# Kernel tuning notes

Hardware: AMD Instinct MI355X
Metric: run time of the kernel (lower is better)

The kernel has to match this reference:

```python
import jax, jax.numpy as jnp
import numpy as np

NUM_NODES = 4096
IN_DIM = 16
HIDDEN = 64
OUT_DIM = 32
HEADS = 4
NEG_SLOPE = 0.2
NEG_INF = -1e9


def _glorot(key, shape):
    fan_in, fan_out = shape[0], shape[-1]
    lim = jnp.sqrt(6.0 / (fan_in + fan_out))
    return jax.random.uniform(key, shape, jnp.float32, -lim, lim)


def setup_inputs() -> dict:
    key = jax.random.key(0)
    ks = jax.random.split(key, 8)
    B = 2
    return {
        "x": jax.random.normal(ks[0], (B, NUM_NODES, IN_DIM), jnp.float32),
        "embedding": _glorot(ks[1], (NUM_NODES, HIDDEN)),
        "W_proj": _glorot(ks[2], (IN_DIM, HIDDEN)),
        "b_proj": jnp.zeros((HIDDEN,), jnp.float32),
        "W1": _glorot(ks[3], (HIDDEN, HIDDEN)),  # heads=4, 16 per head, concat -> 64
        "att1_src": _glorot(ks[4], (HEADS, HIDDEN // HEADS)),
        "att1_dst": _glorot(ks[5], (HEADS, HIDDEN // HEADS)),
        "b1": jnp.zeros((HIDDEN,), jnp.float32),
        "W2": _glorot(ks[6], (HIDDEN, OUT_DIM)),  # heads=4, 8 per head, concat -> 32
        "att2_src": _glorot(ks[7], (HEADS, OUT_DIM // HEADS)),
        "att2_dst": _glorot(jax.random.fold_in(key, 99), (HEADS, OUT_DIM // HEADS)),
        "b2": jnp.zeros((OUT_DIM,), jnp.float32),
    }


def _gat(x, mask, W, a_src, a_dst, b):
    """Dense masked GAT layer. x: [B,N,Fin], mask: [N,N] bool (shared over batch).

    Equivalent to GATConv over edge list tf.where(adj > 0.5): for each target i,
    softmax over neighbors j of LeakyReLU(a_dst.Wh_i + a_src.Wh_j), aggregate Wh_j.
    """
    B, N, _ = x.shape
    H, F = a_src.shape
    h = (x @ W).reshape(B, N, H, F)                       # [B,N,H,F]
    s_src = jnp.einsum('bnhf,hf->bnh', h, a_src)          # per-source score
    s_dst = jnp.einsum('bnhf,hf->bnh', h, a_dst)          # per-target score
    e = s_dst[:, :, None, :] + s_src[:, None, :, :]       # [B,i,j,H]
    e = jnp.where(e > 0, e, NEG_SLOPE * e)                # LeakyReLU(0.2)
    e = jnp.where(mask[None, :, :, None], e, NEG_INF)
    alpha = jax.nn.softmax(e, axis=2)                     # softmax over neighbors j
    out = jnp.einsum('bijh,bjhf->bihf', alpha, h).reshape(B, N, H * F)
    return out + b


def reference(x, embedding, W_proj, b_proj, W1, att1_src, att1_dst, b1,
              W2, att2_src, att2_dst, b2):
    # AdaptiveAdjacency: cosine similarity of l2-normalized node embeddings
    ne = embedding / jnp.linalg.norm(embedding, axis=-1, keepdims=True)
    adj = ne @ ne.T                                       # [N,N], same for all batch
    mask = adj > 0.5                                      # edge set (incl. self-loops)

    h = x @ W_proj + b_proj                               # Dense proj -> hidden
    h = jax.nn.relu(_gat(h, mask, W1, att1_src, att1_dst, b1))
    return _gat(h, mask, W2, att2_src, att2_dst, b2)
```

## Files before the change

### kernel.cpp

```cpp
#include <hip/hip_runtime.h>
#include <hip/hip_bf16.h>
#include <stdint.h>

#define N_NODES 4096
#define BATCH 2

typedef __attribute__((ext_vector_type(8))) short short8v;
typedef __attribute__((ext_vector_type(4))) float f32x4;

#define GLL16(gsrc, ldst) \
    __builtin_amdgcn_global_load_lds((const __attribute__((address_space(1))) void*)(gsrc), \
                                     (__attribute__((address_space(3))) void*)(ldst), 16, 0, 0)

static __device__ inline unsigned short f2bf_rn(float x) {
    unsigned u = __float_as_uint(x);
    unsigned r = (u + 0x7FFFu + ((u >> 16) & 1u)) >> 16;
    return (unsigned short)r;
}
static __device__ inline float bf2f(unsigned short b) {
    return __uint_as_float(((unsigned)b) << 16);
}
static __device__ inline float rl(float v, int k) {
    return __uint_as_float(__builtin_amdgcn_readlane(__float_as_uint(v), k));
}

__global__ __launch_bounds__(64) void norm_kernel(const float* __restrict__ emb,
                                                  unsigned short* __restrict__ hi,
                                                  unsigned short* __restrict__ lo) {
    int row = blockIdx.x;
    int l = threadIdx.x;
    float v = emb[row * 64 + l];
    float s = v * v;
#pragma unroll
    for (int m = 32; m >= 1; m >>= 1) s += __shfl_xor(s, m);
    float nv = v / sqrtf(s);
    unsigned short h = f2bf_rn(nv);
    unsigned short lw = f2bf_rn(nv - bf2f(h));
    hi[row * 64 + l] = h;
    lo[row * 64 + l] = lw;
}

__global__ __launch_bounds__(256) void adj_mfma_kernel(
        const unsigned short* __restrict__ hi, const unsigned short* __restrict__ lo,
        unsigned long long* __restrict__ mask) {
    __shared__ unsigned short Ah[128 * 64];
    __shared__ unsigned short Al[128 * 64];
    __shared__ unsigned short Bh[128 * 64];
    __shared__ unsigned short Bl[128 * 64];
    int t = threadIdx.x;
    int w = t >> 6, l = t & 63;
    int i0 = blockIdx.y * 128, j0 = blockIdx.x * 128;

    int cr = l >> 3;
    int slot = (l & 7) ^ cr;
#pragma unroll
    for (int q = 0; q < 4; ++q) {
        int lr = w * 32 + q * 8;
        size_t ga = (size_t)(i0 + lr + cr) * 64 + slot * 8;
        size_t gb = (size_t)(j0 + lr + cr) * 64 + slot * 8;
        GLL16(hi + ga, &Ah[lr * 64]);
        GLL16(lo + ga, &Al[lr * 64]);
        GLL16(hi + gb, &Bh[lr * 64]);
        GLL16(lo + gb, &Bl[lr * 64]);
    }
    __syncthreads();

    int fr = l & 15;
    int s0 = l >> 4;
    int r7 = l & 7;
    short8v aH[2][2], aL[2][2];
#pragma unroll
    for (int rt = 0; rt < 2; ++rt) {
        int base = (w * 32 + rt * 16 + fr) * 64;
        aH[rt][0] = *(const short8v*)&Ah[base + ((s0 ^ r7) << 3)];
        aH[rt][1] = *(const short8v*)&Ah[base + (((s0 + 4) ^ r7) << 3)];
        aL[rt][0] = *(const short8v*)&Al[base + ((s0 ^ r7) << 3)];
        aL[rt][1] = *(const short8v*)&Al[base + (((s0 + 4) ^ r7) << 3)];
    }

    f32x4 acc[2][8];
#pragma unroll
    for (int rt = 0; rt < 2; ++rt)
#pragma unroll
        for (int js = 0; js < 8; ++js) acc[rt][js] = (f32x4){0.f, 0.f, 0.f, 0.f};

#pragma unroll
    for (int js = 0; js < 8; ++js) {
        int bbase = (js * 16 + fr) * 64;
        short8v bH0 = *(const short8v*)&Bh[bbase + ((s0 ^ r7) << 3)];
        short8v bH1 = *(const short8v*)&Bh[bbase + (((s0 + 4) ^ r7) << 3)];
        short8v bL0 = *(const short8v*)&Bl[bbase + ((s0 ^ r7) << 3)];
        short8v bL1 = *(const short8v*)&Bl[bbase + (((s0 + 4) ^ r7) << 3)];
#pragma unroll
        for (int rt = 0; rt < 2; ++rt) {
            f32x4 a = acc[rt][js];
            a = __builtin_amdgcn_mfma_f32_16x16x32_bf16(aH[rt][0], bH0, a, 0, 0, 0);
            a = __builtin_amdgcn_mfma_f32_16x16x32_bf16(aH[rt][1], bH1, a, 0, 0, 0);
            a = __builtin_amdgcn_mfma_f32_16x16x32_bf16(aH[rt][0], bL0, a, 0, 0, 0);
            a = __builtin_amdgcn_mfma_f32_16x16x32_bf16(aH[rt][1], bL1, a, 0, 0, 0);
            a = __builtin_amdgcn_mfma_f32_16x16x32_bf16(aL[rt][0], bH0, a, 0, 0, 0);
            a = __builtin_amdgcn_mfma_f32_16x16x32_bf16(aL[rt][1], bH1, a, 0, 0, 0);
            acc[rt][js] = a;
        }
    }

    int shift = ((l & 15) >> 2) * 16;
    int r = l & 3;
#pragma unroll
    for (int rt = 0; rt < 2; ++rt) {
#pragma unroll
        for (int ws_ = 0; ws_ < 2; ++ws_) {
            unsigned long long w64 = 0;
#pragma unroll
            for (int js2 = 0; js2 < 4; ++js2) {
                f32x4 a = acc[rt][ws_ * 4 + js2];
                unsigned long long b0 = __ballot(a[0] > 0.5f);
                unsigned long long b1 = __ballot(a[1] > 0.5f);
                unsigned long long b2 = __ballot(a[2] > 0.5f);
                unsigned long long b3 = __ballot(a[3] > 0.5f);
                unsigned long long sel = r == 0 ? b0 : r == 1 ? b1 : r == 2 ? b2 : b3;
                w64 |= ((sel >> shift) & 0xFFFFULL) << (js2 * 16);
            }
            if (l < 16)
                mask[(size_t)(i0 + w * 32 + rt * 16 + l) * 64 + blockIdx.x * 2 + ws_] = w64;
        }
    }
}

__global__ __launch_bounds__(256) void feat1_kernel(
        const float* __restrict__ x, const float* __restrict__ Wp,
        const float* __restrict__ bp, const float* __restrict__ W1,
        const float* __restrict__ a1s, const float* __restrict__ a1d,
        float* __restrict__ h1out, float* __restrict__ ssrc, float* __restrict__ sdst) {
    int w = threadIdx.x >> 6, l = threadIdx.x & 63;
    int row0 = blockIdx.x * 16 + w * 4;

    float xv[4];
#pragma unroll
    for (int r = 0; r < 4; ++r) xv[r] = x[(size_t)(row0 + r) * 16 + (l & 15)];

    float h0[4];
    float bpv = bp[l];
#pragma unroll
    for (int r = 0; r < 4; ++r) h0[r] = bpv;
#pragma unroll
    for (int k = 0; k < 16; ++k) {
        float wk = Wp[k * 64 + l];
#pragma unroll
        for (int r = 0; r < 4; ++r) h0[r] += rl(xv[r], k) * wk;
    }

    float h1[4] = {0.f, 0.f, 0.f, 0.f};
#pragma unroll
    for (int k = 0; k < 64; ++k) {
        float wk = W1[k * 64 + l];
#pragma unroll
        for (int r = 0; r < 4; ++r) h1[r] += rl(h0[r], k) * wk;
    }

    float as_ = a1s[l], ad_ = a1d[l];
#pragma unroll
    for (int r = 0; r < 4; ++r) {
        h1out[(size_t)(row0 + r) * 64 + l] = h1[r];
        float ps = h1[r] * as_, pd = h1[r] * ad_;
#pragma unroll
        for (int m = 8; m >= 1; m >>= 1) {
            ps += __shfl_xor(ps, m);
            pd += __shfl_xor(pd, m);
        }
        if ((l & 15) == 0) {
            ssrc[(size_t)(row0 + r) * 4 + (l >> 4)] = ps;
            sdst[(size_t)(row0 + r) * 4 + (l >> 4)] = pd;
        }
    }
}

__global__ __launch_bounds__(64) void agg1_fused_kernel(
        const float* __restrict__ h1, const float* __restrict__ ssrc,
        const float* __restrict__ sdst, const unsigned long long* __restrict__ mask,
        const float* __restrict__ b1, const float* __restrict__ W2,
        const float* __restrict__ a2s, const float* __restrict__ a2d,
        float* __restrict__ h2out, float* __restrict__ s2s, float* __restrict__ s2d) {
    int row = blockIdx.x;
    int i = row & (N_NODES - 1);
    int bN = row - i;
    int t = threadIdx.x;
    int hh = t >> 4;

    float sd = sdst[(size_t)row * 4 + hh];
    unsigned long long myword = mask[(size_t)i * 64 + t];

    float m = -1e30f, denom = 0.f, acc = 0.f;
    unsigned long long nz = __ballot(myword != 0ULL);
    while (nz) {
        int lw = __ffsll(nz) - 1;
        nz &= nz - 1;
        unsigned long long wbits = __shfl(myword, lw);
        while (wbits) {
            int bpos = __ffsll(wbits) - 1;
            wbits &= wbits - 1;
            int j = (lw << 6) + bpos;
            float e = sd + ssrc[(size_t)(bN + j) * 4 + hh];
            e = e > 0.f ? e : 0.2f * e;
            float mn = fmaxf(m, e);
            float cf = __expf(m - mn);
            float wg = __expf(e - mn);
            float hv = h1[(size_t)(bN + j) * 64 + t];
            denom = denom * cf + wg;
            acc = acc * cf + wg * hv;
            m = mn;
        }
    }
    float o = fmaxf(acc / denom + b1[t], 0.f);

    int l2 = t & 31;
    float acc2 = 0.f;
#pragma unroll
    for (int k = 0; k < 64; ++k) acc2 += rl(o, k) * W2[k * 32 + l2];

    float ps = acc2 * a2s[l2], pd = acc2 * a2d[l2];
#pragma unroll
    for (int mm = 4; mm >= 1; mm >>= 1) {
        ps += __shfl_xor(ps, mm);
        pd += __shfl_xor(pd, mm);
    }
    if (t < 32) {
        h2out[(size_t)row * 32 + t] = acc2;
        if ((t & 7) == 0) {
            s2s[(size_t)row * 4 + (t >> 3)] = ps;
            s2d[(size_t)row * 4 + (t >> 3)] = pd;
        }
    }
}

template <int HID, int F, int RELU>
__global__ __launch_bounds__(64) void gat_agg_kernel(
        const float* __restrict__ hfeat, const float* __restrict__ ssrc,
        const float* __restrict__ sdst, const unsigned long long* __restrict__ mask,
        const float* __restrict__ bias, float* __restrict__ out) {
    int row = blockIdx.x;
    int i = row & (N_NODES - 1);
    int bN = row - i;
    int t = threadIdx.x;
    int tt = t & (HID - 1);
    int hh = tt / F;

    float sd = sdst[(size_t)row * 4 + hh];
    unsigned long long myword = mask[(size_t)i * 64 + t];

    float m = -1e30f, denom = 0.f, acc = 0.f;
    unsigned long long nz = __ballot(myword != 0ULL);
    while (nz) {
        int lw = __ffsll(nz) - 1;
        nz &= nz - 1;
        unsigned long long wbits = __shfl(myword, lw);
        while (wbits) {
            int bpos = __ffsll(wbits) - 1;
            wbits &= wbits - 1;
            int j = (lw << 6) + bpos;
            float e = sd + ssrc[(size_t)(bN + j) * 4 + hh];
            e = e > 0.f ? e : 0.2f * e;
            float mn = fmaxf(m, e);
            float cf = __expf(m - mn);
            float wg = __expf(e - mn);
            float hv = hfeat[(size_t)(bN + j) * HID + tt];
            denom = denom * cf + wg;
            acc = acc * cf + wg * hv;
            m = mn;
        }
    }
    float o = acc / denom + bias[tt];
    if (RELU) o = fmaxf(o, 0.f);
    if (t < HID) out[(size_t)row * HID + tt] = o;
}

extern "C" void kernel_launch(void* const* d_in, const int* in_sizes, int n_in,
                              void* d_out, int out_size, void* d_ws, size_t ws_size,
                              hipStream_t stream) {
    const float* x   = (const float*)d_in[0];
    const float* emb = (const float*)d_in[1];
    const float* Wp  = (const float*)d_in[2];
    const float* bp  = (const float*)d_in[3];
    const float* W1  = (const float*)d_in[4];
    const float* a1s = (const float*)d_in[5];
    const float* a1d = (const float*)d_in[6];
    const float* b1  = (const float*)d_in[7];
    const float* W2  = (const float*)d_in[8];
    const float* a2s = (const float*)d_in[9];
    const float* a2d = (const float*)d_in[10];
    const float* b2  = (const float*)d_in[11];

    const int ROWS = BATCH * N_NODES;

    char* w = (char*)d_ws;
    unsigned short* ne_hi = (unsigned short*)w;  w += (size_t)N_NODES * 64 * 2;
    unsigned short* ne_lo = (unsigned short*)w;  w += (size_t)N_NODES * 64 * 2;
    unsigned long long* mask = (unsigned long long*)w; w += (size_t)N_NODES * 64 * 8;
    float* h1  = (float*)w;                      w += (size_t)ROWS * 64 * 4;
    float* s1s = (float*)w;                      w += (size_t)ROWS * 4 * 4;
    float* s1d = (float*)w;                      w += (size_t)ROWS * 4 * 4;
    float* h2  = (float*)w;                      w += (size_t)ROWS * 32 * 4;
    float* s2s = (float*)w;                      w += (size_t)ROWS * 4 * 4;
    float* s2d = (float*)w;                      w += (size_t)ROWS * 4 * 4;

    norm_kernel<<<dim3(N_NODES), dim3(64), 0, stream>>>(emb, ne_hi, ne_lo);
    adj_mfma_kernel<<<dim3(32, 32), dim3(256), 0, stream>>>(ne_hi, ne_lo, mask);
    feat1_kernel<<<dim3(ROWS / 16), dim3(256), 0, stream>>>(
        x, Wp, bp, W1, a1s, a1d, h1, s1s, s1d);
    agg1_fused_kernel<<<dim3(ROWS), dim3(64), 0, stream>>>(
        h1, s1s, s1d, mask, b1, W2, a2s, a2d, h2, s2s, s2d);
    gat_agg_kernel<32, 8, 0><<<dim3(ROWS), dim3(64), 0, stream>>>(
        h2, s2s, s2d, mask, b2, (float*)d_out);
}
```

Baseline: 39.06 us.

## Fuse normalization into adjacency kernel and co-launch feature projection blocks

```diff
diff --git a/kernel.cpp b/kernel.cpp
--- a/kernel.cpp
+++ b/kernel.cpp
@@ -6,11 +6,8 @@
 #define BATCH 2
 
 typedef __attribute__((ext_vector_type(8))) short short8v;
+typedef __attribute__((ext_vector_type(4))) unsigned short ushort4v;
 typedef __attribute__((ext_vector_type(4))) float f32x4;
-
-#define GLL16(gsrc, ldst) \
-    __builtin_amdgcn_global_load_lds((const __attribute__((address_space(1))) void*)(gsrc), \
-                                     (__attribute__((address_space(3))) void*)(ldst), 16, 0, 0)
 
 static __device__ inline unsigned short f2bf_rn(float x) {
     unsigned u = __float_as_uint(x);
@@ -24,167 +21,170 @@
     return __uint_as_float(__builtin_amdgcn_readlane(__float_as_uint(v), k));
 }
 
-__global__ __launch_bounds__(64) void norm_kernel(const float* __restrict__ emb,
-                                                  unsigned short* __restrict__ hi,
-                                                  unsigned short* __restrict__ lo) {
-    int row = blockIdx.x;
-    int l = threadIdx.x;
-    float v = emb[row * 64 + l];
-    float s = v * v;
-#pragma unroll
-    for (int m = 32; m >= 1; m >>= 1) s += __shfl_xor(s, m);
-    float nv = v / sqrtf(s);
-    unsigned short h = f2bf_rn(nv);
-    unsigned short lw = f2bf_rn(nv - bf2f(h));
-    hi[row * 64 + l] = h;
-    lo[row * 64 + l] = lw;
-}
-
-__global__ __launch_bounds__(256) void adj_mfma_kernel(
-        const unsigned short* __restrict__ hi, const unsigned short* __restrict__ lo,
-        unsigned long long* __restrict__ mask) {
+__global__ __launch_bounds__(256) void k1_kernel(
+        const float* __restrict__ emb, unsigned long long* __restrict__ mask,
+        const float* __restrict__ x, const float* __restrict__ Wp,
+        const float* __restrict__ bp, const float* __restrict__ W1,
+        const float* __restrict__ a1s, const float* __restrict__ a1d,
+        float* __restrict__ h1out, float* __restrict__ ssrc, float* __restrict__ sdst) {
     __shared__ unsigned short Ah[128 * 64];
     __shared__ unsigned short Al[128 * 64];
     __shared__ unsigned short Bh[128 * 64];
     __shared__ unsigned short Bl[128 * 64];
     int t = threadIdx.x;
-    int w = t >> 6, l = t & 63;
-    int i0 = blockIdx.y * 128, j0 = blockIdx.x * 128;
-
-    int cr = l >> 3;
-    int slot = (l & 7) ^ cr;
-#pragma unroll
-    for (int q = 0; q < 4; ++q) {
-        int lr = w * 32 + q * 8;
-        size_t ga = (size_t)(i0 + lr + cr) * 64 + slot * 8;
-        size_t gb = (size_t)(j0 + lr + cr) * 64 + slot * 8;
-        GLL16(hi + ga, &Ah[lr * 64]);
-        GLL16(lo + ga, &Al[lr * 64]);
-        GLL16(hi + gb, &Bh[lr * 64]);
-        GLL16(lo + gb, &Bl[lr * 64]);
-    }
-    __syncthreads();
-
-    int fr = l & 15;
-    int s0 = l >> 4;
-    int r7 = l & 7;
-    short8v aH[2][2], aL[2][2];
-#pragma unroll
-    for (int rt = 0; rt < 2; ++rt) {
-        int base = (w * 32 + rt * 16 + fr) * 64;
-        aH[rt][0] = *(const short8v*)&Ah[base + ((s0 ^ r7) << 3)];
-        aH[rt][1] = *(const short8v*)&Ah[base + (((s0 + 4) ^ r7) << 3)];
-        aL[rt][0] = *(const short8v*)&Al[base + ((s0 ^ r7) << 3)];
-        aL[rt][1] = *(const short8v*)&Al[base + (((s0 + 4) ^ r7) << 3)];
-    }
-
-    f32x4 acc[2][8];
-#pragma unroll
-    for (int rt = 0; rt < 2; ++rt)
-#pragma unroll
-        for (int js = 0; js < 8; ++js) acc[rt][js] = (f32x4){0.f, 0.f, 0.f, 0.f};
-
-#pragma unroll
-    for (int js = 0; js < 8; ++js) {
-        int bbase = (js * 16 + fr) * 64;
-        short8v bH0 = *(const short8v*)&Bh[bbase + ((s0 ^ r7) << 3)];
-        short8v bH1 = *(const short8v*)&Bh[bbase + (((s0 + 4) ^ r7) << 3)];
-        short8v bL0 = *(const short8v*)&Bl[bbase + ((s0 ^ r7) << 3)];
-        short8v bL1 = *(const short8v*)&Bl[bbase + (((s0 + 4) ^ r7) << 3)];
+
+    if (blockIdx.x < 1024) {
+        int bi = blockIdx.x >> 5, bj = blockIdx.x & 31;
+        int i0 = bi * 128, j0 = bj * 128;
+        int w = t >> 6, l = t & 63;
+
+        int l16 = t & 15;
+        int s8 = l16 >> 1, hf = l16 & 1;
+#pragma unroll
+        for (int it = 0; it < 8; ++it) {
+            int r = it * 16 + (t >> 4);
+            float4 av = *(const float4*)&emb[(size_t)(i0 + r) * 64 + l16 * 4];
+            float4 bv = *(const float4*)&emb[(size_t)(j0 + r) * 64 + l16 * 4];
+            float sa = av.x * av.x + av.y * av.y + av.z * av.z + av.w * av.w;
+            float sb = bv.x * bv.x + bv.y * bv.y + bv.z * bv.z + bv.w * bv.w;
+#pragma unroll
+            for (int m = 8; m >= 1; m >>= 1) {
+                sa += __shfl_xor(sa, m);
+                sb += __shfl_xor(sb, m);
+            }
+            float ia = 1.f / sqrtf(sa), ib = 1.f / sqrtf(sb);
+            float a0 = av.x * ia, a1 = av.y * ia, a2 = av.z * ia, a3 = av.w * ia;
+            float b0 = bv.x * ib, b1 = bv.y * ib, b2 = bv.z * ib, b3 = bv.w * ib;
+            ushort4v ah = {f2bf_rn(a0), f2bf_rn(a1), f2bf_rn(a2), f2bf_rn(a3)};
+            ushort4v bh = {f2bf_rn(b0), f2bf_rn(b1), f2bf_rn(b2), f2bf_rn(b3)};
+            ushort4v al = {f2bf_rn(a0 - bf2f(ah.x)), f2bf_rn(a1 - bf2f(ah.y)),
+                           f2bf_rn(a2 - bf2f(ah.z)), f2bf_rn(a3 - bf2f(ah.w))};
+            ushort4v bl = {f2bf_rn(b0 - bf2f(bh.x)), f2bf_rn(b1 - bf2f(bh.y)),
+                           f2bf_rn(b2 - bf2f(bh.z)), f2bf_rn(b3 - bf2f(bh.w))};
+            int si = r * 64 + ((s8 ^ (r & 7)) << 3) + hf * 4;
+            *(ushort4v*)&Ah[si] = ah;
+            *(ushort4v*)&Al[si] = al;
+            *(ushort4v*)&Bh[si] = bh;
+            *(ushort4v*)&Bl[si] = bl;
+        }
+        __syncthreads();
+
+        int fr = l & 15;
+        int s0 = l >> 4;
+        int r7 = l & 7;
+        short8v aH[2][2], aL[2][2];
 #pragma unroll
         for (int rt = 0; rt < 2; ++rt) {
-            f32x4 a = acc[rt][js];
-            a = __builtin_amdgcn_mfma_f32_16x16x32_bf16(aH[rt][0], bH0, a, 0, 0, 0);
-            a = __builtin_amdgcn_mfma_f32_16x16x32_bf16(aH[rt][1], bH1, a, 0, 0, 0);
-            a = __builtin_amdgcn_mfma_f32_16x16x32_bf16(aH[rt][0], bL0, a, 0, 0, 0);
-            a = __builtin_amdgcn_mfma_f32_16x16x32_bf16(aH[rt][1], bL1, a, 0, 0, 0);
-            a = __builtin_amdgcn_mfma_f32_16x16x32_bf16(aL[rt][0], bH0, a, 0, 0, 0);
-            a = __builtin_amdgcn_mfma_f32_16x16x32_bf16(aL[rt][1], bH1, a, 0, 0, 0);
-            acc[rt][js] = a;
-        }
-    }
-
-    int shift = ((l & 15) >> 2) * 16;
-    int r = l & 3;
-#pragma unroll
-    for (int rt = 0; rt < 2; ++rt) {
-#pragma unroll
-        for (int ws_ = 0; ws_ < 2; ++ws_) {
-            unsigned long long w64 = 0;
-#pragma unroll
-            for (int js2 = 0; js2 < 4; ++js2) {
-                f32x4 a = acc[rt][ws_ * 4 + js2];
-                unsigned long long b0 = __ballot(a[0] > 0.5f);
-                unsigned long long b1 = __ballot(a[1] > 0.5f);
-                unsigned long long b2 = __ballot(a[2] > 0.5f);
-                unsigned long long b3 = __ballot(a[3] > 0.5f);
-                unsigned long long sel = r == 0 ? b0 : r == 1 ? b1 : r == 2 ? b2 : b3;
-                w64 |= ((sel >> shift) & 0xFFFFULL) << (js2 * 16);
-            }
-            if (l < 16)
-                mask[(size_t)(i0 + w * 32 + rt * 16 + l) * 64 + blockIdx.x * 2 + ws_] = w64;
-        }
-    }
-}
-
-__global__ __launch_bounds__(256) void feat1_kernel(
-        const float* __restrict__ x, const float* __restrict__ Wp,
-        const float* __restrict__ bp, const float* __restrict__ W1,
-        const float* __restrict__ a1s, const float* __restrict__ a1d,
-        float* __restrict__ h1out, float* __restrict__ ssrc, float* __restrict__ sdst) {
-    int w = threadIdx.x >> 6, l = threadIdx.x & 63;
-    int row0 = blockIdx.x * 16 + w * 4;
-
-    float xv[4];
-#pragma unroll
-    for (int r = 0; r < 4; ++r) xv[r] = x[(size_t)(row0 + r) * 16 + (l & 15)];
-
-    float h0[4];
-    float bpv = bp[l];
-#pragma unroll
-    for (int r = 0; r < 4; ++r) h0[r] = bpv;
-#pragma unroll
-    for (int k = 0; k < 16; ++k) {
-        float wk = Wp[k * 64 + l];
-#pragma unroll
-        for (int r = 0; r < 4; ++r) h0[r] += rl(xv[r], k) * wk;
-    }
-
-    float h1[4] = {0.f, 0.f, 0.f, 0.f};
-#pragma unroll
-    for (int k = 0; k < 64; ++k) {
-        float wk = W1[k * 64 + l];
-#pragma unroll
-        for (int r = 0; r < 4; ++r) h1[r] += rl(h0[r], k) * wk;
-    }
-
-    float as_ = a1s[l], ad_ = a1d[l];
-#pragma unroll
-    for (int r = 0; r < 4; ++r) {
-        h1out[(size_t)(row0 + r) * 64 + l] = h1[r];
-        float ps = h1[r] * as_, pd = h1[r] * ad_;
-#pragma unroll
-        for (int m = 8; m >= 1; m >>= 1) {
-            ps += __shfl_xor(ps, m);
-            pd += __shfl_xor(pd, m);
-        }
-        if ((l & 15) == 0) {
-            ssrc[(size_t)(row0 + r) * 4 + (l >> 4)] = ps;
-            sdst[(size_t)(row0 + r) * 4 + (l >> 4)] = pd;
-        }
-    }
-}
-
-__global__ __launch_bounds__(64) void agg1_fused_kernel(
+            int base = (w * 32 + rt * 16 + fr) * 64;
+            aH[rt][0] = *(const short8v*)&Ah[base + ((s0 ^ r7) << 3)];
+            aH[rt][1] = *(const short8v*)&Ah[base + (((s0 + 4) ^ r7) << 3)];
+            aL[rt][0] = *(const short8v*)&Al[base + ((s0 ^ r7) << 3)];
+            aL[rt][1] = *(const short8v*)&Al[base + (((s0 + 4) ^ r7) << 3)];
+        }
+
+        f32x4 acc[2][8];
+#pragma unroll
+        for (int rt = 0; rt < 2; ++rt)
+#pragma unroll
+            for (int js = 0; js < 8; ++js) acc[rt][js] = (f32x4){0.f, 0.f, 0.f, 0.f};
+
+#pragma unroll
+        for (int js = 0; js < 8; ++js) {
+            int bbase = (js * 16 + fr) * 64;
+            short8v bH0 = *(const short8v*)&Bh[bbase + ((s0 ^ r7) << 3)];
+            short8v bH1 = *(const short8v*)&Bh[bbase + (((s0 + 4) ^ r7) << 3)];
+            short8v bL0 = *(const short8v*)&Bl[bbase + ((s0 ^ r7) << 3)];
+            short8v bL1 = *(const short8v*)&Bl[bbase + (((s0 + 4) ^ r7) << 3)];
+#pragma unroll
+            for (int rt = 0; rt < 2; ++rt) {
+                f32x4 a = acc[rt][js];
+                a = __builtin_amdgcn_mfma_f32_16x16x32_bf16(aH[rt][0], bH0, a, 0, 0, 0);
+                a = __builtin_amdgcn_mfma_f32_16x16x32_bf16(aH[rt][1], bH1, a, 0, 0, 0);
+                a = __builtin_amdgcn_mfma_f32_16x16x32_bf16(aH[rt][0], bL0, a, 0, 0, 0);
+                a = __builtin_amdgcn_mfma_f32_16x16x32_bf16(aH[rt][1], bL1, a, 0, 0, 0);
+                a = __builtin_amdgcn_mfma_f32_16x16x32_bf16(aL[rt][0], bH0, a, 0, 0, 0);
+                a = __builtin_amdgcn_mfma_f32_16x16x32_bf16(aL[rt][1], bH1, a, 0, 0, 0);
+                acc[rt][js] = a;
+            }
+        }
+
+        int shift = ((l & 15) >> 2) * 16;
+        int r = l & 3;
+#pragma unroll
+        for (int rt = 0; rt < 2; ++rt) {
+#pragma unroll
+            for (int ws_ = 0; ws_ < 2; ++ws_) {
+                unsigned long long w64 = 0;
+#pragma unroll
+                for (int js2 = 0; js2 < 4; ++js2) {
+                    f32x4 a = acc[rt][ws_ * 4 + js2];
+                    unsigned long long c0 = __ballot(a[0] > 0.5f);
+                    unsigned long long c1 = __ballot(a[1] > 0.5f);
+                    unsigned long long c2 = __ballot(a[2] > 0.5f);
+                    unsigned long long c3 = __ballot(a[3] > 0.5f);
+                    unsigned long long sel = r == 0 ? c0 : r == 1 ? c1 : r == 2 ? c2 : c3;
+                    w64 |= ((sel >> shift) & 0xFFFFULL) << (js2 * 16);
+                }
+                if (l < 16)
+                    mask[(size_t)(i0 + w * 32 + rt * 16 + l) * 64 + bj * 2 + ws_] = w64;
+            }
+        }
+    } else {
+        int b = blockIdx.x - 1024;
+        int w = t >> 6, l = t & 63;
+        int row0 = b * 32 + w * 8;
+
+        float xv[8];
+#pragma unroll
+        for (int r = 0; r < 8; ++r) xv[r] = x[(size_t)(row0 + r) * 16 + (l & 15)];
+
+        float h0[8];
+        float bpv = bp[l];
+#pragma unroll
+        for (int r = 0; r < 8; ++r) h0[r] = bpv;
+#pragma unroll
+        for (int k = 0; k < 16; ++k) {
+            float wk = Wp[k * 64 + l];
+#pragma unroll
+            for (int r = 0; r < 8; ++r) h0[r] += rl(xv[r], k) * wk;
+        }
+
+        float h1[8] = {0.f, 0.f, 0.f, 0.f, 0.f, 0.f, 0.f, 0.f};
+#pragma unroll
+        for (int k = 0; k < 64; ++k) {
+            float wk = W1[k * 64 + l];
+#pragma unroll
+            for (int r = 0; r < 8; ++r) h1[r] += rl(h0[r], k) * wk;
+        }
+
+        float as_ = a1s[l], ad_ = a1d[l];
+#pragma unroll
+        for (int r = 0; r < 8; ++r) {
+            h1out[(size_t)(row0 + r) * 64 + l] = h1[r];
+            float ps = h1[r] * as_, pd = h1[r] * ad_;
+#pragma unroll
+            for (int m = 8; m >= 1; m >>= 1) {
+                ps += __shfl_xor(ps, m);
+                pd += __shfl_xor(pd, m);
+            }
+            if ((l & 15) == 0) {
+                ssrc[(size_t)(row0 + r) * 4 + (l >> 4)] = ps;
+                sdst[(size_t)(row0 + r) * 4 + (l >> 4)] = pd;
+            }
+        }
+    }
+}
+
+__global__ __launch_bounds__(256) void agg1_fused_kernel(
         const float* __restrict__ h1, const float* __restrict__ ssrc,
         const float* __restrict__ sdst, const unsigned long long* __restrict__ mask,
         const float* __restrict__ b1, const float* __restrict__ W2,
         const float* __restrict__ a2s, const float* __restrict__ a2d,
         float* __restrict__ h2out, float* __restrict__ s2s, float* __restrict__ s2d) {
-    int row = blockIdx.x;
+    int row = blockIdx.x * 4 + (threadIdx.x >> 6);
     int i = row & (N_NODES - 1);
     int bN = row - i;
-    int t = threadIdx.x;
+    int t = threadIdx.x & 63;
     int hh = t >> 4;
 
     float sd = sdst[(size_t)row * 4 + hh];
@@ -233,17 +233,16 @@
     }
 }
 
-template <int HID, int F, int RELU>
-__global__ __launch_bounds__(64) void gat_agg_kernel(
+__global__ __launch_bounds__(256) void agg2_kernel(
         const float* __restrict__ hfeat, const float* __restrict__ ssrc,
         const float* __restrict__ sdst, const unsigned long long* __restrict__ mask,
         const float* __restrict__ bias, float* __restrict__ out) {
-    int row = blockIdx.x;
+    int row = blockIdx.x * 4 + (threadIdx.x >> 6);
     int i = row & (N_NODES - 1);
     int bN = row - i;
-    int t = threadIdx.x;
-    int tt = t & (HID - 1);
-    int hh = tt / F;
+    int t = threadIdx.x & 63;
+    int tt = t & 31;
+    int hh = tt >> 3;
 
     float sd = sdst[(size_t)row * 4 + hh];
     unsigned long long myword = mask[(size_t)i * 64 + t];
@@ -263,15 +262,14 @@
             float mn = fmaxf(m, e);
             float cf = __expf(m - mn);
             float wg = __expf(e - mn);
-            float hv = hfeat[(size_t)(bN + j) * HID + tt];
+            float hv = hfeat[(size_t)(bN + j) * 32 + tt];
             denom = denom * cf + wg;
             acc = acc * cf + wg * hv;
             m = mn;
         }
     }
     float o = acc / denom + bias[tt];
-    if (RELU) o = fmaxf(o, 0.f);
-    if (t < HID) out[(size_t)row * HID + tt] = o;
+    if (t < 32) out[(size_t)row * 32 + tt] = o;
 }
 
 extern "C" void kernel_launch(void* const* d_in, const int* in_sizes, int n_in,
@@ -293,8 +291,6 @@
     const int ROWS = BATCH * N_NODES;
 
     char* w = (char*)d_ws;
-    unsigned short* ne_hi = (unsigned short*)w;  w += (size_t)N_NODES * 64 * 2;
-    unsigned short* ne_lo = (unsigned short*)w;  w += (size_t)N_NODES * 64 * 2;
     unsigned long long* mask = (unsigned long long*)w; w += (size_t)N_NODES * 64 * 8;
     float* h1  = (float*)w;                      w += (size_t)ROWS * 64 * 4;
     float* s1s = (float*)w;                      w += (size_t)ROWS * 4 * 4;
@@ -303,12 +299,10 @@
     float* s2s = (float*)w;                      w += (size_t)ROWS * 4 * 4;
     float* s2d = (float*)w;                      w += (size_t)ROWS * 4 * 4;
 
-    norm_kernel<<<dim3(N_NODES), dim3(64), 0, stream>>>(emb, ne_hi, ne_lo);
-    adj_mfma_kernel<<<dim3(32, 32), dim3(256), 0, stream>>>(ne_hi, ne_lo, mask);
-    feat1_kernel<<<dim3(ROWS / 16), dim3(256), 0, stream>>>(
-        x, Wp, bp, W1, a1s, a1d, h1, s1s, s1d);
-    agg1_fused_kernel<<<dim3(ROWS), dim3(64), 0, stream>>>(
+    k1_kernel<<<dim3(1024 + 256), dim3(256), 0, stream>>>(
+        emb, mask, x, Wp, bp, W1, a1s, a1d, h1, s1s, s1d);
+    agg1_fused_kernel<<<dim3(ROWS / 4), dim3(256), 0, stream>>>(
         h1, s1s, s1d, mask, b1, W2, a2s, a2d, h2, s2s, s2d);
-    gat_agg_kernel<32, 8, 0><<<dim3(ROWS), dim3(64), 0, stream>>>(
+    agg2_kernel<<<dim3(ROWS / 4), dim3(256), 0, stream>>>(
         h2, s2s, s2d, mask, b2, (float*)d_out);
 }
```

New measurement: 40.61 us. 4.0% more time.
